# Performance work log

Hardware: AMD Instinct MI355X
Metric: run time of the kernel (lower is better)

Reference implementation:

```python
import jax, jax.numpy as jnp
import numpy as np

B, L, DIN, H, E, K = 64, 256, 768, 64, 8, 2
S = 16  # sqrt(L): token<->feature grid side
LOSS_COEF = 1e-2


def gelu(x):
    return jax.nn.gelu(x, approximate=False)  # torch nn.GELU (exact erf)


def cv_squared(v):
    v = v.astype(jnp.float32)
    return jnp.var(v, ddof=1) / (jnp.mean(v) ** 2 + 1e-10)


def setup_inputs() -> dict:
    key = jax.random.key(0)
    ks = jax.random.split(key, 16)
    rn = lambda k, shape, s=0.02: jax.random.normal(k, shape, jnp.float32) * s
    lap = jnp.array([[0., 1., 0.], [1., -4., 1.], [0., 1., 0.]], jnp.float32)
    return {
        "x": jax.random.normal(ks[0], (B, L, DIN), jnp.float32),
        "dte": jax.random.normal(ks[1], (B, L, DIN), jnp.float32),
        "w_gate": rn(ks[2], (L, E), 1.0),
        "W_exp": rn(ks[3], (E, DIN, H)), "b_exp": jnp.zeros((E, H), jnp.float32),
        "W_sh": rn(ks[4], (DIN, H)), "b_sh": jnp.zeros((H,), jnp.float32),
        "ln_g": jnp.ones((H,), jnp.float32), "ln_b": jnp.zeros((H,), jnp.float32),
        "W_px": rn(ks[5], (H, 2 * H)), "b_px": jnp.zeros((2 * H,), jnp.float32),
        "conv_sh": jnp.tile(lap[None, None], (H, 1, 1, 1)),  # depthwise Laplacian [H,1,3,3]
        "W_pxx": rn(ks[6], (H, H)), "b_pxx": jnp.zeros((H,), jnp.float32),
        "W_dte": rn(ks[7], (H, H)), "b_dte": jnp.zeros((H,), jnp.float32),
        "W_dteall": rn(ks[8], (H, H)), "b_dteall": jnp.zeros((H,), jnp.float32),
        "W_rgb": rn(ks[9], (DIN, H)), "b_rgb": jnp.zeros((H,), jnp.float32),
        "W_fx": rn(ks[10], (H, H)), "b_fx": jnp.zeros((H,), jnp.float32),
        "W_fmod": rn(ks[11], (H, H)), "b_fmod": jnp.zeros((H,), jnp.float32),
        "W_fxx": rn(ks[12], (H, H)), "b_fxx": jnp.zeros((H,), jnp.float32),
    }


def reference(x, dte, w_gate, W_exp, b_exp, W_sh, b_sh, ln_g, ln_b, W_px, b_px,
              conv_sh, W_pxx, b_pxx, W_dte, b_dte, W_dteall, b_dteall,
              W_rgb, b_rgb, W_fx, b_fx, W_fmod, b_fmod, W_fxx, b_fxx):
    # ---- top-k gating (clean logits; noisy_gating=False / eval) ----
    logits = dte.mean(-1) @ w_gate                     # [B,E]
    topv, topi = jax.lax.top_k(logits, K)
    topg = jax.nn.softmax(topv, axis=1)
    gates = jnp.zeros_like(logits).at[jnp.arange(B)[:, None], topi].set(topg)
    importance = gates.sum(0)
    load = (gates > 0).sum(0).astype(jnp.float32)
    loss = LOSS_COEF * (cv_squared(importance) + cv_squared(load))
    # ---- sparse dispatch / expert Linear / weighted combine (dense-equivalent) ----
    y = jnp.einsum('be,bld,edh->blh', gates, dte, W_exp) + (gates @ b_exp)[:, None, :]
    # ---- shared expert Linear + Shared block ----
    sh = dte @ W_sh + b_sh                             # [B,L,H]
    shortcut = sh
    t = (sh - sh.mean(-1, keepdims=True)) * jax.lax.rsqrt(sh.var(-1, keepdims=True) + 1e-6)
    t = t * ln_g + ln_b
    t = t @ W_px + b_px                                # [B,L,2H]
    t1, t2 = t[..., :H], t[..., H:]
    f = t1.transpose(0, 2, 1).reshape(B, H, S, S)      # token2feature
    f = jax.lax.conv_general_dilated(f, conv_sh, (1, 1), 'SAME', feature_group_count=H)
    t1 = f.reshape(B, H, L).transpose(0, 2, 1)         # feature2token
    sh = (gelu(t1) * t2) @ W_pxx + b_pxx + shortcut
    # ---- combine MoE and shared streams ----
    dte_tok = (y @ W_dte + b_dte) + (sh @ W_dteall + b_dteall)
    rgb_tok = x @ W_rgb + b_rgb
    # ---- Fusion (its self.norm was overwritten to GELU; token<->feature round-trip is identity) ----
    shortcut = rgb_tok
    a = gelu(rgb_tok) @ W_fx + b_fx
    m = gelu(dte_tok) @ W_fmod + b_fmod
    out = (gelu(m) * a) @ W_fxx + b_fxx + shortcut     # [B,L,H]
    return out, loss
```

## Files before the change

kernel.cpp:

```cpp
#include <hip/hip_runtime.h>
#include <math.h>

typedef unsigned short u16;
typedef unsigned int u32;
typedef __attribute__((ext_vector_type(8))) short bf16x8;
typedef __attribute__((ext_vector_type(4))) float f32x4;


__device__ __forceinline__ float bf2f(u16 u) {
    union { u32 i; float f; } x; x.i = ((u32)u) << 16; return x.f;
}
__device__ __forceinline__ u16 f2bf(float f) {
    union { float f; u32 i; } x; x.f = f;
    u32 i = x.i;
    return (u16)((i + 0x7fffu + ((i >> 16) & 1u)) >> 16);
}
__device__ __forceinline__ u32 pack2(float a, float b) {
    return (u32)f2bf(a) | ((u32)f2bf(b) << 16);
}
__device__ __forceinline__ float wsum(float v) {
    #pragma unroll
    for (int o = 1; o < 64; o <<= 1) v += __shfl_xor(v, o, 64);
    return v;
}
__device__ __forceinline__ float gelu_f(float x) {
    return 0.5f * x * (1.0f + erff(x * 0.70710678118654752440f));
}

__global__ __launch_bounds__(256) void k_gate_part(const float* __restrict__ dte,
                                                   const float* __restrict__ w_gate,
                                                   float* __restrict__ partial) {
    __shared__ float dmeanS[64];
    int p = blockIdx.x, tid = threadIdx.x, w = tid >> 6, lane = tid & 63;
    for (int i = 0; i < 16; i++) {
        int l = w * 16 + i;
        const float* pr = dte + ((size_t)p * 64 + l) * 768;
        float s = 0.f;
        #pragma unroll
        for (int j = 0; j < 3; j++) {
            float4 v = *(const float4*)(pr + (lane + j * 64) * 4);
            s += v.x + v.y + v.z + v.w;
        }
        s = wsum(s);
        if (lane == 0) dmeanS[l] = s * (1.f / 768.f);
    }
    __syncthreads();
    if (w == 0) {
        float dm = dmeanS[lane];
        int wl = (p & 3) * 64 + lane;
        #pragma unroll
        for (int e = 0; e < 8; e++) {
            float s = wsum(dm * w_gate[wl * 8 + e]);
            if (lane == 0) partial[p * 8 + e] = s;
        }
    }
}

__global__ __launch_bounds__(256) void k_gate_fin(const float* __restrict__ partial,
                                                  const float* __restrict__ b_exp,
                                                  int* __restrict__ topi,
                                                  float* __restrict__ topg,
                                                  float* __restrict__ bias_y,
                                                  float* __restrict__ loss_out) {
    __shared__ float gS[64 * 8];
    __shared__ int i0S[64], i1S[64];
    __shared__ float g0S[64], g1S[64];
    int tid = threadIdx.x;
    if (tid < 64) {
        float lg[8];
        #pragma unroll
        for (int e = 0; e < 8; e++)
            lg[e] = partial[(tid * 4 + 0) * 8 + e] + partial[(tid * 4 + 1) * 8 + e] +
                    partial[(tid * 4 + 2) * 8 + e] + partial[(tid * 4 + 3) * 8 + e];
        int i0 = 0; float v0 = lg[0];
        #pragma unroll
        for (int e = 1; e < 8; e++) if (lg[e] > v0) { v0 = lg[e]; i0 = e; }
        int i1 = -1; float v1 = -1e30f;
        #pragma unroll
        for (int e = 0; e < 8; e++) if (e != i0 && lg[e] > v1) { v1 = lg[e]; i1 = e; }
        if (i1 < 0) i1 = (i0 + 1) & 7;
        float e2 = expf(v1 - v0);
        float g0 = 1.f / (1.f + e2);
        float g1 = e2 / (1.f + e2);
        #pragma unroll
        for (int e = 0; e < 8; e++) gS[tid * 8 + e] = 0.f;
        gS[tid * 8 + i0] = g0;
        gS[tid * 8 + i1] = g1;
        i0S[tid] = i0; i1S[tid] = i1; g0S[tid] = g0; g1S[tid] = g1;
        topi[tid * 2] = i0; topi[tid * 2 + 1] = i1;
        topg[tid * 2] = g0; topg[tid * 2 + 1] = g1;
    }
    __syncthreads();
    for (int idx = tid; idx < 4096; idx += 256) {
        int b = idx >> 6, h = idx & 63;
        bias_y[idx] = g0S[b] * b_exp[i0S[b] * 64 + h] + g1S[b] * b_exp[i1S[b] * 64 + h];
    }
    if (tid < 64) {
        float g[8];
        #pragma unroll
        for (int e = 0; e < 8; e++) g[e] = gS[tid * 8 + e];
        float imp[8], ld[8];
        #pragma unroll
        for (int e = 0; e < 8; e++) {
            imp[e] = wsum(g[e]);
            ld[e]  = wsum(g[e] > 0.f ? 1.f : 0.f);
        }
        if (tid == 0) {
            float l = 0.f;
            {
                float s = 0.f;
                #pragma unroll
                for (int e = 0; e < 8; e++) s += imp[e];
                float mn = s / 8.f, v = 0.f;
                #pragma unroll
                for (int e = 0; e < 8; e++) { float d = imp[e] - mn; v += d * d; }
                l += (v / 7.f) / (mn * mn + 1e-10f);
            }
            {
                float s = 0.f;
                #pragma unroll
                for (int e = 0; e < 8; e++) s += ld[e];
                float mn = s / 8.f, v = 0.f;
                #pragma unroll
                for (int e = 0; e < 8; e++) { float d = ld[e] - mn; v += d * d; }
                l += (v / 7.f) / (mn * mn + 1e-10f);
            }
            loss_out[0] = 0.01f * l;
        }
    }
}

__global__ __launch_bounds__(256) void k_gemm3(const float* __restrict__ dte,
                                               const float* __restrict__ x,
                                               const float* __restrict__ W_sh,
                                               const float* __restrict__ b_sh,
                                               const float* __restrict__ W_exp,
                                               const int* __restrict__ topi,
                                               const float* __restrict__ topg,
                                               const float* __restrict__ bias_y,
                                               const float* __restrict__ W_rgb,
                                               const float* __restrict__ b_rgb,
                                               float* __restrict__ buf_sh,
                                               u16* __restrict__ buf_y,
                                               float* __restrict__ out_rgb) {
    __shared__ u16 As[64 * 72];
    __shared__ u16 Wt[64 * 72];
    int bid = blockIdx.x;
    int kind, row0;
    if (bid < 512) { kind = bid & 1; row0 = (bid >> 1) * 64; }
    else           { kind = 2;       row0 = (bid - 512) * 64; }
    int b = row0 >> 8;
    int tid = threadIdx.x, wv = tid >> 6, lane = tid & 63;
    int m = lane & 15, quad = lane >> 4;

    const float* A = (kind == 2) ? x : dte;
    const float* W0 = (kind == 2) ? W_rgb : W_sh;
    const float* W1 = W0;
    float g0 = 0.f, g1 = 0.f;
    if (kind == 1) {
        W0 = W_exp + (size_t)topi[2 * b] * 49152;
        W1 = W_exp + (size_t)topi[2 * b + 1] * 49152;
        g0 = topg[2 * b]; g1 = topg[2 * b + 1];
    }

    float4 pa[2][2];
    float  pw[16];
    const int a_r  = tid >> 3;
    const int a_k8 = (tid & 7) * 8;
    const int w_n  = tid & 63;
    const int w_k0 = (tid >> 6) * 16;

    auto loadA = [&](int kc) {
        #pragma unroll
        for (int j = 0; j < 2; j++) {
            const float* src = A + (size_t)(row0 + a_r + j * 32) * 768 + kc * 64 + a_k8;
            pa[j][0] = *(const float4*)(src);
            pa[j][1] = *(const float4*)(src + 4);
        }
    };
    auto loadW = [&](int kc) {
        if (kind == 1) {
            #pragma unroll
            for (int j = 0; j < 16; j++) {
                size_t off = (size_t)(kc * 64 + w_k0 + j) * 64 + w_n;
                pw[j] = g0 * W0[off] + g1 * W1[off];
            }
        } else {
            #pragma unroll
            for (int j = 0; j < 16; j++)
                pw[j] = W0[(size_t)(kc * 64 + w_k0 + j) * 64 + w_n];
        }
    };
    auto stageLDS = [&]() {
        #pragma unroll
        for (int j = 0; j < 2; j++) {
            uint4 d;
            d.x = pack2(pa[j][0].x, pa[j][0].y);
            d.y = pack2(pa[j][0].z, pa[j][0].w);
            d.z = pack2(pa[j][1].x, pa[j][1].y);
            d.w = pack2(pa[j][1].z, pa[j][1].w);
            *(uint4*)&As[(a_r + j * 32) * 72 + a_k8] = d;
        }
        uint4 d0, d1;
        d0.x = pack2(pw[0],  pw[1]);  d0.y = pack2(pw[2],  pw[3]);
        d0.z = pack2(pw[4],  pw[5]);  d0.w = pack2(pw[6],  pw[7]);
        d1.x = pack2(pw[8],  pw[9]);  d1.y = pack2(pw[10], pw[11]);
        d1.z = pack2(pw[12], pw[13]); d1.w = pack2(pw[14], pw[15]);
        *(uint4*)&Wt[w_n * 72 + w_k0]     = d0;
        *(uint4*)&Wt[w_n * 72 + w_k0 + 8] = d1;
    };

    f32x4 acc0 = {0.f, 0.f, 0.f, 0.f}, acc1 = acc0, acc2 = acc0, acc3 = acc0;

    loadA(0); loadW(0);
    for (int kc = 0; kc < 12; kc++) {
        __syncthreads();
        stageLDS();
        __syncthreads();
        if (kc < 11) { loadA(kc + 1); loadW(kc + 1); }
        const int ar = (wv * 16 + m) * 72;
        bf16x8 a0 = *(const bf16x8*)&As[ar + quad * 8];
        bf16x8 a1 = *(const bf16x8*)&As[ar + 32 + quad * 8];
        #pragma unroll
        for (int t = 0; t < 4; t++) {
            const int br = (t * 16 + m) * 72;
            bf16x8 b0 = *(const bf16x8*)&Wt[br + quad * 8];
            bf16x8 b1 = *(const bf16x8*)&Wt[br + 32 + quad * 8];
            f32x4* accp = (t == 0) ? &acc0 : (t == 1) ? &acc1 : (t == 2) ? &acc2 : &acc3;
            *accp = __builtin_amdgcn_mfma_f32_16x16x32_bf16(a0, b0, *accp, 0, 0, 0);
            *accp = __builtin_amdgcn_mfma_f32_16x16x32_bf16(a1, b1, *accp, 0, 0, 0);
        }
    }

    f32x4 accs[4] = {acc0, acc1, acc2, acc3};
    #pragma unroll
    for (int t = 0; t < 4; t++) {
        int col = t * 16 + m;
        float bias;
        if (kind == 0)      bias = b_sh[col];
        else if (kind == 1) bias = bias_y[b * 64 + col];
        else                bias = b_rgb[col];
        #pragma unroll
        for (int i = 0; i < 4; i++) {
            int r = row0 + wv * 16 + quad * 4 + i;
            float val = accs[t][i] + bias;
            if (kind == 0)      buf_sh[(size_t)r * 64 + col] = val;
            else if (kind == 1) buf_y[(size_t)r * 64 + col] = f2bf(val);
            else                out_rgb[(size_t)r * 64 + col] = val;
        }
    }
}

__global__ __launch_bounds__(256) void k_lnpx(const float* __restrict__ buf_sh,
                                              const float* __restrict__ ln_g,
                                              const float* __restrict__ ln_b,
                                              const float* __restrict__ W_px,
                                              const float* __restrict__ b_px,
                                              u16* __restrict__ t1, u16* __restrict__ t2) {
    __shared__ float T[32 * 68];
    __shared__ float Wpx[8192];
    int r0 = blockIdx.x * 32;
    int tid = threadIdx.x, w = tid >> 6, lane = tid & 63;
    #pragma unroll
    for (int j = 0; j < 8; j++) {
        int e4 = tid + j * 256;
        *(float4*)(Wpx + e4 * 4) = *(const float4*)(W_px + e4 * 4);
    }
    float lnG = ln_g[lane], lnB = ln_b[lane];
    for (int i = 0; i < 8; i++) {
        int l = w * 8 + i;
        float v = buf_sh[(size_t)(r0 + l) * 64 + lane];
        float mean = wsum(v) * (1.f / 64.f);
        float d = v - mean;
        float var = wsum(d * d) * (1.f / 64.f);
        T[l * 68 + lane] = d * rsqrtf(var + 1e-6f) * lnG + lnB;
    }
    __syncthreads();
    int rg = tid >> 4, cg = tid & 15;
    float acc1[2][4] = {}, acc2[2][4] = {};
    const float* tr = T + rg * 2 * 68;
    #pragma unroll 4
    for (int kk = 0; kk < 64; kk++) {
        float a0 = tr[kk], a1 = tr[68 + kk];
        float4 w1 = *(const float4*)(Wpx + kk * 128 + cg * 4);
        float4 w2 = *(const float4*)(Wpx + kk * 128 + 64 + cg * 4);
        acc1[0][0] += a0 * w1.x; acc1[0][1] += a0 * w1.y; acc1[0][2] += a0 * w1.z; acc1[0][3] += a0 * w1.w;
        acc1[1][0] += a1 * w1.x; acc1[1][1] += a1 * w1.y; acc1[1][2] += a1 * w1.z; acc1[1][3] += a1 * w1.w;
        acc2[0][0] += a0 * w2.x; acc2[0][1] += a0 * w2.y; acc2[0][2] += a0 * w2.z; acc2[0][3] += a0 * w2.w;
        acc2[1][0] += a1 * w2.x; acc2[1][1] += a1 * w2.y; acc2[1][2] += a1 * w2.z; acc2[1][3] += a1 * w2.w;
    }
    float4 b1 = *(const float4*)(b_px + cg * 4);
    float4 b2 = *(const float4*)(b_px + 64 + cg * 4);
    #pragma unroll
    for (int i = 0; i < 2; i++) {
        int r = r0 + rg * 2 + i;
        u32* d1 = (u32*)(t1 + (size_t)r * 64 + cg * 4);
        d1[0] = pack2(acc1[i][0] + b1.x, acc1[i][1] + b1.y);
        d1[1] = pack2(acc1[i][2] + b1.z, acc1[i][3] + b1.w);
        u32* d2 = (u32*)(t2 + (size_t)r * 64 + cg * 4);
        d2[0] = pack2(acc2[i][0] + b2.x, acc2[i][1] + b2.y);
        d2[1] = pack2(acc2[i][2] + b2.z, acc2[i][3] + b2.w);
    }
}

__global__ __launch_bounds__(256) void k_tail(const u16* __restrict__ t1,
                                              const u16* __restrict__ t2,
                                              const float* __restrict__ conv_sh,
                                              const float* __restrict__ W_pxx,
                                              const float* __restrict__ b_pxx,
                                              const float* __restrict__ buf_sh,
                                              const u16* __restrict__ buf_y,
                                              const float* __restrict__ W_dte,
                                              const float* __restrict__ b_dte,
                                              const float* __restrict__ W_dteall,
                                              const float* __restrict__ b_dteall,
                                              const float* __restrict__ W_fx,
                                              const float* __restrict__ b_fx,
                                              const float* __restrict__ W_fmod,
                                              const float* __restrict__ b_fmod,
                                              const float* __restrict__ W_fxx,
                                              const float* __restrict__ b_fxx,
                                              float* __restrict__ out) {
    __shared__ float C0[16 * 68];
    __shared__ float GA[16 * 68];
    __shared__ float SH1[16 * 68];
    __shared__ float GM[16 * 68];
    __shared__ u16   Ybh[16 * 72];
    __shared__ float WL[2][4096];
    int r0 = blockIdx.x * 16;
    int tid = threadIdx.x, w = tid >> 6, lane = tid & 63;
    int rg = tid >> 4, cg = tid & 15;

    float4 wbuf[4];
    auto wload = [&](const float* Wsrc) {
        #pragma unroll
        for (int j = 0; j < 4; j++)
            wbuf[j] = *(const float4*)(Wsrc + (tid + j * 256) * 4);
    };
    auto wstore = [&](int half) {
        #pragma unroll
        for (int j = 0; j < 4; j++)
            *(float4*)(&WL[half][(tid + j * 256) * 4]) = wbuf[j];
    };

    wload(W_pxx);
    float4 rsv;
    {
        uint2 v = *(const uint2*)(buf_y + (size_t)(r0 + rg) * 64 + cg * 4);
        *(uint2*)(&Ybh[rg * 72 + cg * 4]) = v;
    }
    {
        rsv = *(const float4*)(out + (size_t)(r0 + rg) * 64 + cg * 4);
        GA[rg * 68 + cg * 4 + 0] = gelu_f(rsv.x);
        GA[rg * 68 + cg * 4 + 1] = gelu_f(rsv.y);
        GA[rg * 68 + cg * 4 + 2] = gelu_f(rsv.z);
        GA[rg * 68 + cg * 4 + 3] = gelu_f(rsv.w);
    }
    {
        float c0 = conv_sh[lane * 9 + 0], c1 = conv_sh[lane * 9 + 1], c2 = conv_sh[lane * 9 + 2];
        float c3 = conv_sh[lane * 9 + 3], c4 = conv_sh[lane * 9 + 4], c5 = conv_sh[lane * 9 + 5];
        float c6 = conv_sh[lane * 9 + 6], c7 = conv_sh[lane * 9 + 7], c8 = conv_sh[lane * 9 + 8];
        #pragma unroll
        for (int i = 0; i < 4; i++) {
            int l = w * 4 + i;
            int gr = r0 + l;
            int pix = gr & 255, ii = pix >> 4, jj = pix & 15;
            const u16* p = t1 + (size_t)gr * 64 + lane;
            float c = c4 * bf2f(p[0]);
            if (ii > 0) {
                c += c1 * bf2f(p[-1024]);
                if (jj > 0)  c += c0 * bf2f(p[-1024 - 64]);
                if (jj < 15) c += c2 * bf2f(p[-1024 + 64]);
            }
            if (jj > 0)  c += c3 * bf2f(p[-64]);
            if (jj < 15) c += c5 * bf2f(p[64]);
            if (ii < 15) {
                c += c7 * bf2f(p[1024]);
                if (jj > 0)  c += c6 * bf2f(p[1024 - 64]);
                if (jj < 15) c += c8 * bf2f(p[1024 + 64]);
            }
            C0[l * 68 + lane] = gelu_f(c) * bf2f(t2[(size_t)gr * 64 + lane]);
        }
    }
    wstore(0);
    __syncthreads();

    wload(W_dte);
    {
        float acc[4] = {};
        const float* ur = C0 + rg * 68;
        #pragma unroll 8
        for (int kk = 0; kk < 64; kk++) {
            float a0 = ur[kk];
            float4 wv = *(const float4*)(&WL[0][kk * 64 + cg * 4]);
            acc[0] += a0 * wv.x; acc[1] += a0 * wv.y; acc[2] += a0 * wv.z; acc[3] += a0 * wv.w;
        }
        float4 bp = *(const float4*)(b_pxx + cg * 4);
        float4 shv = *(const float4*)(buf_sh + (size_t)(r0 + rg) * 64 + cg * 4);
        *(float4*)(SH1 + rg * 68 + cg * 4) =
            make_float4(acc[0] + bp.x + shv.x, acc[1] + bp.y + shv.y,
                        acc[2] + bp.z + shv.z, acc[3] + bp.w + shv.w);
    }
    wstore(1);
    __syncthreads();

    float accC[4] = {};
    wload(W_dteall);
    {
        const u16* yr = Ybh + rg * 72;
        #pragma unroll 8
        for (int kk = 0; kk < 64; kk++) {
            float y0 = bf2f(yr[kk]);
            float4 wv = *(const float4*)(&WL[1][kk * 64 + cg * 4]);
            accC[0] += y0 * wv.x; accC[1] += y0 * wv.y; accC[2] += y0 * wv.z; accC[3] += y0 * wv.w;
        }
    }
    wstore(0);
    __syncthreads();

    wload(W_fx);
    {
        const float* sr = SH1 + rg * 68;
        #pragma unroll 8
        for (int kk = 0; kk < 64; kk++) {
            float s0 = sr[kk];
            float4 wv = *(const float4*)(&WL[0][kk * 64 + cg * 4]);
            accC[0] += s0 * wv.x; accC[1] += s0 * wv.y; accC[2] += s0 * wv.z; accC[3] += s0 * wv.w;
        }
        float4 bd1 = *(const float4*)(b_dte + cg * 4);
        float4 bd2 = *(const float4*)(b_dteall + cg * 4);
        *(float4*)(GM + rg * 68 + cg * 4) =
            make_float4(gelu_f(accC[0] + bd1.x + bd2.x), gelu_f(accC[1] + bd1.y + bd2.y),
                        gelu_f(accC[2] + bd1.z + bd2.z), gelu_f(accC[3] + bd1.w + bd2.w));
    }
    wstore(1);
    __syncthreads();

    float accA[4] = {};
    wload(W_fmod);
    {
        const float* ga = GA + rg * 68;
        #pragma unroll 8
        for (int kk = 0; kk < 64; kk++) {
            float a0 = ga[kk];
            float4 wv = *(const float4*)(&WL[1][kk * 64 + cg * 4]);
            accA[0] += a0 * wv.x; accA[1] += a0 * wv.y; accA[2] += a0 * wv.z; accA[3] += a0 * wv.w;
        }
    }
    wstore(0);
    __syncthreads();

    wload(W_fxx);
    {
        float accM[4] = {};
        const float* gm = GM + rg * 68;
        #pragma unroll 8
        for (int kk = 0; kk < 64; kk++) {
            float m0 = gm[kk];
            float4 wv = *(const float4*)(&WL[0][kk * 64 + cg * 4]);
            accM[0] += m0 * wv.x; accM[1] += m0 * wv.y; accM[2] += m0 * wv.z; accM[3] += m0 * wv.w;
        }
        float4 bx = *(const float4*)(b_fx + cg * 4);
        float4 bm = *(const float4*)(b_fmod + cg * 4);
        float a0 = accA[0] + bx.x, a1 = accA[1] + bx.y, a2 = accA[2] + bx.z, a3 = accA[3] + bx.w;
        float m0 = accM[0] + bm.x, m1 = accM[1] + bm.y, m2 = accM[2] + bm.z, m3 = accM[3] + bm.w;
        *(float4*)(C0 + rg * 68 + cg * 4) =
            make_float4(gelu_f(m0) * a0, gelu_f(m1) * a1, gelu_f(m2) * a2, gelu_f(m3) * a3);
    }
    wstore(1);
    __syncthreads();

    {
        float acc[4] = {};
        const float* pr = C0 + rg * 68;
        #pragma unroll 8
        for (int kk = 0; kk < 64; kk++) {
            float p0 = pr[kk];
            float4 wv = *(const float4*)(&WL[1][kk * 64 + cg * 4]);
            acc[0] += p0 * wv.x; acc[1] += p0 * wv.y; acc[2] += p0 * wv.z; acc[3] += p0 * wv.w;
        }
        float4 bo = *(const float4*)(b_fxx + cg * 4);
        *(float4*)(out + (size_t)(r0 + rg) * 64 + cg * 4) =
            make_float4(acc[0] + bo.x + rsv.x, acc[1] + bo.y + rsv.y,
                        acc[2] + bo.z + rsv.z, acc[3] + bo.w + rsv.w);
    }
}

extern "C" void kernel_launch(void* const* d_in, const int* in_sizes, int n_in,
                              void* d_out, int out_size, void* d_ws, size_t ws_size,
                              hipStream_t stream) {
    const float* x       = (const float*)d_in[0];
    const float* dte     = (const float*)d_in[1];
    const float* w_gate  = (const float*)d_in[2];
    const float* W_exp   = (const float*)d_in[3];
    const float* b_exp   = (const float*)d_in[4];
    const float* W_sh    = (const float*)d_in[5];
    const float* b_sh    = (const float*)d_in[6];
    const float* ln_g    = (const float*)d_in[7];
    const float* ln_b    = (const float*)d_in[8];
    const float* W_px    = (const float*)d_in[9];
    const float* b_px    = (const float*)d_in[10];
    const float* conv_sh = (const float*)d_in[11];
    const float* W_pxx   = (const float*)d_in[12];
    const float* b_pxx   = (const float*)d_in[13];
    const float* W_dte   = (const float*)d_in[14];
    const float* b_dte   = (const float*)d_in[15];
    const float* W_dteall= (const float*)d_in[16];
    const float* b_dteall= (const float*)d_in[17];
    const float* W_rgb   = (const float*)d_in[18];
    const float* b_rgb   = (const float*)d_in[19];
    const float* W_fx    = (const float*)d_in[20];
    const float* b_fx    = (const float*)d_in[21];
    const float* W_fmod  = (const float*)d_in[22];
    const float* b_fmod  = (const float*)d_in[23];
    const float* W_fxx   = (const float*)d_in[24];
    const float* b_fxx   = (const float*)d_in[25];

    float* out = (float*)d_out;

    float* wsf    = (float*)d_ws;
    float* partial= wsf;
    int*   topi   = (int*)(wsf + 2048);
    float* topg   = wsf + 2176;
    float* bias_y = wsf + 2304;
    float* buf_sh = wsf + 8192;
    u16*   buf_y  = (u16*)(wsf + 8192 + 1048576);
    u16*   t1     = (u16*)(wsf + 8192 + 1048576 + 524288);
    u16*   t2     = (u16*)(wsf + 8192 + 1048576 + 524288*2);

    hipLaunchKernelGGL(k_gate_part, dim3(256), dim3(256), 0, stream, dte, w_gate, partial);
    hipLaunchKernelGGL(k_gate_fin, dim3(1), dim3(256), 0, stream,
                       partial, b_exp, topi, topg, bias_y, out + 1048576);
    hipLaunchKernelGGL(k_gemm3, dim3(768), dim3(256), 0, stream,
                       dte, x, W_sh, b_sh, W_exp, topi, topg, bias_y, W_rgb, b_rgb,
                       buf_sh, buf_y, out);
    hipLaunchKernelGGL(k_lnpx, dim3(512), dim3(256), 0, stream,
                       buf_sh, ln_g, ln_b, W_px, b_px, t1, t2);
    hipLaunchKernelGGL(k_tail, dim3(1024), dim3(256), 0, stream,
                       t1, t2, conv_sh, W_pxx, b_pxx, buf_sh, buf_y,
                       W_dte, b_dte, W_dteall, b_dteall,
                       W_fx, b_fx, W_fmod, b_fmod, W_fxx, b_fxx, out);

    (void)in_sizes; (void)n_in; (void)out_size; (void)ws_size;
}
```

Before: 258.6 us.

## Stage fusion-kernel weights directly into LDS and batch gate-mean loads

The final fusion kernel now copies each 64x64 weight matrix straight from global memory into shared memory with `global_load_lds`. This replaces the old path of loading into registers and then storing to LDS, which removes the register staging and the extra LDS stores. It also lets loads for later stages be issued earlier, into the alternate buffer. The gate-mean kernel now issues 8 rows of loads before reducing them, to raise memory-level parallelism, and the bf16 conversions use the HIP intrinsics. A risk is that correctness depends on the asynchronous LDS DMA having finished before each barrier-protected read.

```diff
diff --git a/kernel.cpp b/kernel.cpp
--- a/kernel.cpp
+++ b/kernel.cpp
@@ -1,4 +1,5 @@
 #include <hip/hip_runtime.h>
+#include <hip/hip_bf16.h>
 #include <math.h>
 
 typedef unsigned short u16;
@@ -11,12 +12,14 @@
     union { u32 i; float f; } x; x.i = ((u32)u) << 16; return x.f;
 }
 __device__ __forceinline__ u16 f2bf(float f) {
-    union { float f; u32 i; } x; x.f = f;
-    u32 i = x.i;
-    return (u16)((i + 0x7fffu + ((i >> 16) & 1u)) >> 16);
+    union { __hip_bfloat16 h; u16 u; } x;
+    x.h = __float2bfloat16(f);
+    return x.u;
 }
 __device__ __forceinline__ u32 pack2(float a, float b) {
-    return (u32)f2bf(a) | ((u32)f2bf(b) << 16);
+    union { __hip_bfloat162 h; u32 u; } x;
+    x.h = __float22bfloat162_rn(make_float2(a, b));
+    return x.u;
 }
 __device__ __forceinline__ float wsum(float v) {
     #pragma unroll
@@ -32,17 +35,25 @@
                                                    float* __restrict__ partial) {
     __shared__ float dmeanS[64];
     int p = blockIdx.x, tid = threadIdx.x, w = tid >> 6, lane = tid & 63;
-    for (int i = 0; i < 16; i++) {
-        int l = w * 16 + i;
-        const float* pr = dte + ((size_t)p * 64 + l) * 768;
-        float s = 0.f;
-        #pragma unroll
-        for (int j = 0; j < 3; j++) {
-            float4 v = *(const float4*)(pr + (lane + j * 64) * 4);
-            s += v.x + v.y + v.z + v.w;
-        }
-        s = wsum(s);
-        if (lane == 0) dmeanS[l] = s * (1.f / 768.f);
+    #pragma unroll
+    for (int h = 0; h < 2; h++) {
+        float4 v[8][3];
+        #pragma unroll
+        for (int i = 0; i < 8; i++) {
+            const float* pr = dte + ((size_t)p * 64 + w * 16 + h * 8 + i) * 768;
+            #pragma unroll
+            for (int j = 0; j < 3; j++)
+                v[i][j] = *(const float4*)(pr + (lane + j * 64) * 4);
+        }
+        #pragma unroll
+        for (int i = 0; i < 8; i++) {
+            float s = 0.f;
+            #pragma unroll
+            for (int j = 0; j < 3; j++)
+                s += v[i][j].x + v[i][j].y + v[i][j].z + v[i][j].w;
+            s = wsum(s);
+            if (lane == 0) dmeanS[w * 16 + h * 8 + i] = s * (1.f / 768.f);
+        }
     }
     __syncthreads();
     if (w == 0) {
@@ -326,30 +337,30 @@
     __shared__ float SH1[16 * 68];
     __shared__ float GM[16 * 68];
     __shared__ u16   Ybh[16 * 72];
-    __shared__ float WL[2][4096];
+    __shared__ __align__(16) float WL[2][4096];
     int r0 = blockIdx.x * 16;
     int tid = threadIdx.x, w = tid >> 6, lane = tid & 63;
     int rg = tid >> 4, cg = tid & 15;
 
-    float4 wbuf[4];
-    auto wload = [&](const float* Wsrc) {
-        #pragma unroll
-        for (int j = 0; j < 4; j++)
-            wbuf[j] = *(const float4*)(Wsrc + (tid + j * 256) * 4);
+    auto stage_w = [&](const float* __restrict__ Wsrc, int half) {
+        const float* g = Wsrc + w * 1024 + lane * 4;
+        float* l = &WL[half][w * 1024];
+        #pragma unroll
+        for (int j = 0; j < 4; j++) {
+            __builtin_amdgcn_global_load_lds(
+                (const __attribute__((address_space(1))) unsigned int*)(g + j * 256),
+                (__attribute__((address_space(3))) unsigned int*)(l + j * 256),
+                16, 0, 0);
+        }
     };
-    auto wstore = [&](int half) {
-        #pragma unroll
-        for (int j = 0; j < 4; j++)
-            *(float4*)(&WL[half][(tid + j * 256) * 4]) = wbuf[j];
-    };
-
-    wload(W_pxx);
+
+    stage_w(W_pxx, 0);
+
+    stage_w(W_dte, 1);
     float4 rsv;
     {
         uint2 v = *(const uint2*)(buf_y + (size_t)(r0 + rg) * 64 + cg * 4);
         *(uint2*)(&Ybh[rg * 72 + cg * 4]) = v;
-    }
-    {
         rsv = *(const float4*)(out + (size_t)(r0 + rg) * 64 + cg * 4);
         GA[rg * 68 + cg * 4 + 0] = gelu_f(rsv.x);
         GA[rg * 68 + cg * 4 + 1] = gelu_f(rsv.y);
@@ -382,10 +393,8 @@
             C0[l * 68 + lane] = gelu_f(c) * bf2f(t2[(size_t)gr * 64 + lane]);
         }
     }
-    wstore(0);
-    __syncthreads();
-
-    wload(W_dte);
+    __syncthreads();
+
     {
         float acc[4] = {};
         const float* ur = C0 + rg * 68;
@@ -401,11 +410,10 @@
             make_float4(acc[0] + bp.x + shv.x, acc[1] + bp.y + shv.y,
                         acc[2] + bp.z + shv.z, acc[3] + bp.w + shv.w);
     }
-    wstore(1);
     __syncthreads();
 
     float accC[4] = {};
-    wload(W_dteall);
+    stage_w(W_dteall, 0);
     {
         const u16* yr = Ybh + rg * 72;
         #pragma unroll 8
@@ -415,10 +423,9 @@
             accC[0] += y0 * wv.x; accC[1] += y0 * wv.y; accC[2] += y0 * wv.z; accC[3] += y0 * wv.w;
         }
     }
-    wstore(0);
-    __syncthreads();
-
-    wload(W_fx);
+    __syncthreads();
+
+    stage_w(W_fx, 1);
     {
         const float* sr = SH1 + rg * 68;
         #pragma unroll 8
@@ -433,11 +440,10 @@
             make_float4(gelu_f(accC[0] + bd1.x + bd2.x), gelu_f(accC[1] + bd1.y + bd2.y),
                         gelu_f(accC[2] + bd1.z + bd2.z), gelu_f(accC[3] + bd1.w + bd2.w));
     }
-    wstore(1);
     __syncthreads();
 
     float accA[4] = {};
-    wload(W_fmod);
+    stage_w(W_fmod, 0);
     {
         const float* ga = GA + rg * 68;
         #pragma unroll 8
@@ -447,10 +453,9 @@
             accA[0] += a0 * wv.x; accA[1] += a0 * wv.y; accA[2] += a0 * wv.z; accA[3] += a0 * wv.w;
         }
     }
-    wstore(0);
-    __syncthreads();
-
-    wload(W_fxx);
+    __syncthreads();
+
+    stage_w(W_fxx, 1);
     {
         float accM[4] = {};
         const float* gm = GM + rg * 68;
@@ -467,7 +472,6 @@
         *(float4*)(C0 + rg * 68 + cg * 4) =
             make_float4(gelu_f(m0) * a0, gelu_f(m1) * a1, gelu_f(m2) * a2, gelu_f(m3) * a3);
     }
-    wstore(1);
     __syncthreads();
 
     {
```

New measurement: 241.9 us. 1.07x faster.
